# Optimization experiments

Hardware: AMD Instinct MI355X
Metric: run time of the kernel (lower is better)

Reference implementation:

```python
import jax, jax.numpy as jnp
import numpy as np

WIN = (7, 7, 7)
N = WIN[0] * WIN[1] * WIN[2]   # 343 tokens per window
DIM = 192
NH = 6
HD = DIM // NH                  # 32
B = 128                         # batch * num_windows


def _relative_position_index():
    # exact replica of the torch buffer computation
    coords = np.stack(np.meshgrid(np.arange(WIN[0]), np.arange(WIN[1]), np.arange(WIN[2]), indexing='ij'))
    cf = coords.reshape(3, -1)                       # [3, N]
    rel = cf[:, :, None] - cf[:, None, :]            # [3, N, N]
    rel = rel.transpose(1, 2, 0).astype(np.int64)    # [N, N, 3]
    rel[..., 0] += WIN[0] - 1
    rel[..., 1] += WIN[1] - 1
    rel[..., 2] += WIN[2] - 1
    rel[..., 0] *= (2 * WIN[1] - 1) * (2 * WIN[2] - 1)
    rel[..., 1] *= (2 * WIN[2] - 1)
    return rel.sum(-1).astype(np.int32)              # [N, N]


def setup_inputs() -> dict:
    key = jax.random.key(0)
    k = jax.random.split(key, 8)
    table_size = (2 * WIN[0] - 1) * (2 * WIN[1] - 1) * (2 * WIN[2] - 1)  # 2197
    return {
        'x':        jax.random.normal(k[0], (B, N, DIM), jnp.float32),
        'x_1':      jax.random.normal(k[1], (B, N, DIM), jnp.float32),
        'qkv_w':    jax.random.normal(k[2], (3 * DIM, DIM), jnp.float32) * 0.02,
        'qkv_b':    jnp.zeros((3 * DIM,), jnp.float32),
        'proj_w':   jax.random.normal(k[3], (DIM, DIM), jnp.float32) * 0.02,
        'proj_b':   jnp.zeros((DIM,), jnp.float32),
        'rpb_table': jax.random.normal(k[4], (table_size, NH), jnp.float32) * 0.02,
        'rel_idx':  jnp.asarray(_relative_position_index()),
    }


def reference(x, x_1, qkv_w, qkv_b, proj_w, proj_b, rpb_table, rel_idx):
    scale = HD ** -0.5

    def qkv_proj(t):
        # [B, N, 3C] -> [3, B, nH, N, hd]
        q = (t @ qkv_w.T + qkv_b).reshape(B, N, 3, NH, HD).transpose(2, 0, 3, 1, 4)
        return q[0], q[1], q[2]

    qx, kx, vx = qkv_proj(x)
    q1, k1, v1 = qkv_proj(x_1)

    # gathered relative-position bias: [1, nH, N, N]
    bias = rpb_table[rel_idx.reshape(-1)].reshape(N, N, NH).transpose(2, 0, 1)[None]

    def attend(q, k, v):
        a = jnp.einsum('bhnd,bhmd->bhnm', q * scale, k) + bias
        a = jax.nn.softmax(a, axis=-1)
        o = jnp.einsum('bhnm,bhmd->bhnd', a, v).transpose(0, 2, 1, 3).reshape(B, N, DIM)
        return o @ proj_w.T + proj_b

    # cross-modal pairing: q from x with k,v from x_1; q from x_1 with k,v from x
    out = attend(qx, k1, v1)
    out_1 = attend(q1, kx, vx)
    return out, out_1
```

## Files before the change

kernel.cpp:

```cpp
#include <hip/hip_runtime.h>
#include <hip/hip_bf16.h>

#define BW 128
#define NTOK 343
#define DIMC 192
#define NHEAD 6
#define HDIM 32
#define TOK (BW * NTOK)
#define M2 (2 * TOK)
#define NN (NTOK * NTOK)
#define BSTR 344
#define BNN (NTOK * BSTR)
#define QSCALE 0.17677669529663687f
#define LOG2E 1.4426950408889634f

typedef unsigned int uint32;
typedef __attribute__((ext_vector_type(8))) short short8;
typedef __attribute__((ext_vector_type(4))) float f32x4;

__device__ __forceinline__ unsigned short f2bf(float f) {
  uint32 u = __float_as_uint(f);
  u += 0x7fffu + ((u >> 16) & 1u);
  return (unsigned short)(u >> 16);
}

__device__ __forceinline__ uint32 pkpair(float a, float b) {
  __hip_bfloat162 h = __float22bfloat162_rn(make_float2(a, b));
  uint32 u;
  __builtin_memcpy(&u, &h, 4);
  return u;
}

__device__ __forceinline__ uint4 pack8bf(const float4 a, const float4 b) {
  uint4 pk;
  pk.x = pkpair(a.x, a.y);
  pk.y = pkpair(a.z, a.w);
  pk.z = pkpair(b.x, b.y);
  pk.w = pkpair(b.z, b.w);
  return pk;
}

__device__ __forceinline__ float fexp2(float x) {
  float r;
  asm("v_exp_f32 %0, %1" : "=v"(r) : "v"(x));
  return r;
}

__global__ void k_bias(const float* __restrict__ rpb, const int* __restrict__ ridx,
                       float* __restrict__ biasws) {
  const int idx = blockIdx.x * 256 + threadIdx.x;
  if (idx < NN) {
    const int r = ridx[idx];
    const int i = idx / NTOK, j = idx % NTOK;
#pragma unroll
    for (int h = 0; h < NHEAD; ++h)
      biasws[h * BNN + i * BSTR + j] = rpb[r * NHEAD + h] * LOG2E;
  }
}

__global__ __launch_bounds__(256) void k_qkv(const float* __restrict__ x,
                                             const float* __restrict__ x1,
                                             const float* __restrict__ w,
                                             const float* __restrict__ bvec,
                                             unsigned short* __restrict__ qkvo) {
  __shared__ unsigned short Xs[128][200];
  __shared__ unsigned short Ws[64][200];
  const int R0 = blockIdx.x * 128;
  const int s = R0 / TOK;
  const int tokbase = R0 % TOK;
  const float* __restrict__ src = s ? x1 : x;
  const int tid = threadIdx.x;
  const int lane = tid & 63, wv = tid >> 6;
  const int c16 = lane & 15, q4 = lane >> 4;
  const int wr = wv >> 1, wc = wv & 1;

  int bidxv[4], nnv[4];
#pragma unroll
  for (int n = 0; n < 4; ++n) {
    const int tok = tokbase + wr * 64 + n * 16 + c16;
    bidxv[n] = tok / NTOK;
    nnv[n] = tok % NTOK;
  }

  for (int c = tid; c < 128 * 24; c += 256) {
    const int r = c / 24, k8 = (c % 24) * 8;
    const float* p = &src[(size_t)(tokbase + r) * DIMC + k8];
    const float4 a = *reinterpret_cast<const float4*>(p);
    const float4 b = *reinterpret_cast<const float4*>(p + 4);
    *reinterpret_cast<uint4*>(&Xs[r][k8]) = pack8bf(a, b);
  }

  float4 wa[6], wb[6];
#pragma unroll
  for (int i = 0; i < 6; ++i) {
    const int c = tid + i * 256;
    const int r = c / 24, k8 = (c % 24) * 8;
    const float* p = &w[(size_t)(0 * 64 + r) * DIMC + k8];
    wa[i] = *reinterpret_cast<const float4*>(p);
    wb[i] = *reinterpret_cast<const float4*>(p + 4);
  }

  for (int ct = 0; ct < 9; ++ct) {
    __syncthreads();
#pragma unroll
    for (int i = 0; i < 6; ++i) {
      const int c = tid + i * 256;
      const int r = c / 24, k8 = (c % 24) * 8;
      *reinterpret_cast<uint4*>(&Ws[r][k8]) = pack8bf(wa[i], wb[i]);
    }
    __syncthreads();

    if (ct < 8) {
#pragma unroll
      for (int i = 0; i < 6; ++i) {
        const int c = tid + i * 256;
        const int r = c / 24, k8 = (c % 24) * 8;
        const float* p = &w[(size_t)((ct + 1) * 64 + r) * DIMC + k8];
        wa[i] = *reinterpret_cast<const float4*>(p);
        wb[i] = *reinterpret_cast<const float4*>(p + 4);
      }
    }

    const int colbase = ct * 64 + wc * 32;
    f32x4 acc[2][4];
#pragma unroll
    for (int m = 0; m < 2; ++m) {
      const float4 bb = *reinterpret_cast<const float4*>(&bvec[colbase + m * 16 + q4 * 4]);
#pragma unroll
      for (int n = 0; n < 4; ++n) acc[m][n] = f32x4{bb.x, bb.y, bb.z, bb.w};
    }
#pragma unroll
    for (int ks = 0; ks < 6; ++ks) {
      const short8 w0 = *reinterpret_cast<const short8*>(&Ws[wc * 32 + c16][ks * 32 + q4 * 8]);
      const short8 w1 = *reinterpret_cast<const short8*>(&Ws[wc * 32 + 16 + c16][ks * 32 + q4 * 8]);
      short8 xf[4];
#pragma unroll
      for (int n = 0; n < 4; ++n)
        xf[n] = *reinterpret_cast<const short8*>(&Xs[wr * 64 + n * 16 + c16][ks * 32 + q4 * 8]);
#pragma unroll
      for (int n = 0; n < 4; ++n) {
        acc[0][n] = __builtin_amdgcn_mfma_f32_16x16x32_bf16(w0, xf[n], acc[0][n], 0, 0, 0);
        acc[1][n] = __builtin_amdgcn_mfma_f32_16x16x32_bf16(w1, xf[n], acc[1][n], 0, 0, 0);
      }
    }

    const int t = ct / 3;
    const float qs = (t == 0) ? (QSCALE * LOG2E) : 1.0f;
#pragma unroll
    for (int m = 0; m < 2; ++m) {
      const int col0 = colbase + m * 16 + q4 * 4;
      const int h = (col0 - t * DIMC) / HDIM;
      const int d0 = col0 & (HDIM - 1);
      const size_t hb = ((size_t)(s * 3 + t) * BW) * NHEAD + h;
#pragma unroll
      for (int n = 0; n < 4; ++n) {
        const f32x4 a = acc[m][n];
        uint2 pk;
        pk.x = pkpair(a[0] * qs, a[1] * qs);
        pk.y = pkpair(a[2] * qs, a[3] * qs);
        const size_t ob = ((hb + (size_t)bidxv[n] * NHEAD) * NTOK + nnv[n]) * HDIM + d0;
        *reinterpret_cast<uint2*>(&qkvo[ob]) = pk;
      }
    }
  }
}

__global__ __launch_bounds__(256) void k_attn(const __hip_bfloat16* __restrict__ qkvi,
                                              const float* __restrict__ biasws,
                                              __hip_bfloat16* __restrict__ Ows) {
  __shared__ unsigned short Ks[352][40];
  __shared__ unsigned short Vt[32][360];
  const int bid = blockIdx.x;
  const int h = bid / (2 * BW);
  const int sb = bid % (2 * BW);
  const int s = sb >> 7;
  const int b = sb & 127;
  const int so = 1 - s;
  const size_t qbase = (((size_t)(s * 3 + 0) * BW + b) * NHEAD + h) * (size_t)NTOK * HDIM;
  const size_t kbase = (((size_t)(so * 3 + 1) * BW + b) * NHEAD + h) * (size_t)NTOK * HDIM;
  const size_t vbase = (((size_t)(so * 3 + 2) * BW + b) * NHEAD + h) * (size_t)NTOK * HDIM;
  const unsigned short* __restrict__ qp = (const unsigned short*)qkvi;
  unsigned short* __restrict__ op = (unsigned short*)Ows;
  const float* __restrict__ bh = biasws + (size_t)h * BNN;
  const int tid = threadIdx.x;

  for (int idx = tid; idx < 352 * 4; idx += 256) {
    const int n = idx >> 2, d0 = (idx & 3) * 8;
    uint4 v = {0u, 0u, 0u, 0u};
    if (n < NTOK) v = *reinterpret_cast<const uint4*>(qp + kbase + (size_t)n * HDIM + d0);
    *reinterpret_cast<uint4*>(&Ks[n][d0]) = v;
  }
  for (int idx = tid; idx < NTOK * 4; idx += 256) {
    const int n = idx >> 2, d0 = (idx & 3) * 8;
    const uint4 v = *reinterpret_cast<const uint4*>(qp + vbase + (size_t)n * HDIM + d0);
    const unsigned short* ep = reinterpret_cast<const unsigned short*>(&v);
#pragma unroll
    for (int e = 0; e < 8; ++e) Vt[d0 + e][n] = ep[e];
  }
  for (int idx = tid; idx < 32 * 9; idx += 256) Vt[idx / 9][NTOK + idx % 9] = 0;
  __syncthreads();

  const int lane = tid & 63, w = tid >> 6;
  const int c16 = lane & 15, q4 = lane >> 4;
  const bool loSel = (q4 < 2);

  for (int qt = w; qt < 22; qt += 4) {
    const int iq = qt * 16 + c16;
    const int iqc = (iq < NTOK) ? iq : NTOK - 1;
    const short8 qf = *reinterpret_cast<const short8*>(qp + qbase + (size_t)iqc * HDIM + q4 * 8);
    const float* brow = bh + (size_t)iqc * BSTR;

    f32x4 o0 = {0.f, 0.f, 0.f, 0.f}, o1 = {0.f, 0.f, 0.f, 0.f};
    float mA, sumA;

    {
      f32x4 acc[12];
#pragma unroll
      for (int kt = 0; kt < 12; ++kt) {
        const float4 bv = *reinterpret_cast<const float4*>(brow + kt * 16 + q4 * 4);
        acc[kt] = f32x4{bv.x, bv.y, bv.z, bv.w};
      }
#pragma unroll
      for (int kt = 0; kt < 12; ++kt) {
        const short8 kf = *reinterpret_cast<const short8*>(&Ks[kt * 16 + c16][q4 * 8]);
        acc[kt] = __builtin_amdgcn_mfma_f32_16x16x32_bf16(kf, qf, acc[kt], 0, 0, 0);
      }
      float m = acc[0][0];
#pragma unroll
      for (int kt = 0; kt < 12; ++kt)
#pragma unroll
        for (int r = 0; r < 4; ++r) m = fmaxf(m, acc[kt][r]);
      m = fmaxf(m, __shfl_xor(m, 16, 64));
      m = fmaxf(m, __shfl_xor(m, 32, 64));
      mA = m;
      float sum = 0.f;
#pragma unroll
      for (int kt = 0; kt < 12; ++kt)
#pragma unroll
        for (int r = 0; r < 4; ++r) {
          const float p = fexp2(acc[kt][r] - m);
          acc[kt][r] = p;
          sum += p;
        }
      sumA = sum;

#pragma unroll
      for (int ks = 0; ks < 6; ++ks) {
        uint4 pw;
        pw.x = pkpair(acc[2 * ks][0], acc[2 * ks][1]);
        pw.y = pkpair(acc[2 * ks][2], acc[2 * ks][3]);
        pw.z = pkpair(acc[2 * ks + 1][0], acc[2 * ks + 1][1]);
        pw.w = pkpair(acc[2 * ks + 1][2], acc[2 * ks + 1][3]);
        const short8 pf = *reinterpret_cast<const short8*>(&pw);
        const uint2 v0lo = *reinterpret_cast<const uint2*>(&Vt[c16][ks * 32 + q4 * 4]);
        const uint2 v0hi = *reinterpret_cast<const uint2*>(&Vt[c16][ks * 32 + 16 + q4 * 4]);
        const uint2 v1lo = *reinterpret_cast<const uint2*>(&Vt[16 + c16][ks * 32 + q4 * 4]);
        const uint2 v1hi = *reinterpret_cast<const uint2*>(&Vt[16 + c16][ks * 32 + 16 + q4 * 4]);
        uint4 vw0, vw1;
        vw0.x = v0lo.x; vw0.y = v0lo.y; vw0.z = v0hi.x; vw0.w = v0hi.y;
        vw1.x = v1lo.x; vw1.y = v1lo.y; vw1.z = v1hi.x; vw1.w = v1hi.y;
        const short8 v0 = *reinterpret_cast<const short8*>(&vw0);
        const short8 v1 = *reinterpret_cast<const short8*>(&vw1);
        o0 = __builtin_amdgcn_mfma_f32_16x16x32_bf16(pf, v0, o0, 0, 0, 0);
        o1 = __builtin_amdgcn_mfma_f32_16x16x32_bf16(pf, v1, o1, 0, 0, 0);
      }
    }

    float rinv;
    {
      f32x4 acc[10];
#pragma unroll
      for (int k2 = 0; k2 < 10; ++k2) {
        const int kt = 12 + k2;
        const int jb = (kt < 21) ? (kt * 16 + q4 * 4) : (336 + (loSel ? q4 * 4 : 0));
        const float4 bv = *reinterpret_cast<const float4*>(brow + jb);
        acc[k2] = f32x4{bv.x, bv.y, bv.z, bv.w};
      }
#pragma unroll
      for (int k2 = 0; k2 < 10; ++k2) {
        const short8 kf = *reinterpret_cast<const short8*>(&Ks[(12 + k2) * 16 + c16][q4 * 8]);
        acc[k2] = __builtin_amdgcn_mfma_f32_16x16x32_bf16(kf, qf, acc[k2], 0, 0, 0);
      }
#pragma unroll
      for (int r = 0; r < 4; ++r)
        if (q4 * 4 + r >= 7) acc[9][r] = -1e30f;

      float m = acc[0][0];
#pragma unroll
      for (int k2 = 0; k2 < 10; ++k2)
#pragma unroll
        for (int r = 0; r < 4; ++r) m = fmaxf(m, acc[k2][r]);
      m = fmaxf(m, __shfl_xor(m, 16, 64));
      m = fmaxf(m, __shfl_xor(m, 32, 64));
      m = fmaxf(m, mA);
      const float alpha = fexp2(mA - m);

      float sum = 0.f;
#pragma unroll
      for (int k2 = 0; k2 < 10; ++k2)
#pragma unroll
        for (int r = 0; r < 4; ++r) {
          const float p = fexp2(acc[k2][r] - m);
          acc[k2][r] = p;
          sum += p;
        }
      float lanesum = sumA * alpha + sum;
      lanesum += __shfl_xor(lanesum, 16, 64);
      lanesum += __shfl_xor(lanesum, 32, 64);
      rinv = 1.f / lanesum;

      float alphar[4];
#pragma unroll
      for (int r = 0; r < 4; ++r) alphar[r] = __shfl(alpha, q4 * 4 + r, 64);
#pragma unroll
      for (int r = 0; r < 4; ++r) {
        o0[r] *= alphar[r];
        o1[r] *= alphar[r];
      }

#pragma unroll
      for (int ks = 6; ks < 11; ++ks) {
        const int k2 = 2 * (ks - 6);
        uint4 pw;
        pw.x = pkpair(acc[k2][0], acc[k2][1]);
        pw.y = pkpair(acc[k2][2], acc[k2][3]);
        pw.z = pkpair(acc[k2 + 1][0], acc[k2 + 1][1]);
        pw.w = pkpair(acc[k2 + 1][2], acc[k2 + 1][3]);
        const short8 pf = *reinterpret_cast<const short8*>(&pw);
        const uint2 v0lo = *reinterpret_cast<const uint2*>(&Vt[c16][ks * 32 + q4 * 4]);
        const uint2 v0hi = *reinterpret_cast<const uint2*>(&Vt[c16][ks * 32 + 16 + q4 * 4]);
        const uint2 v1lo = *reinterpret_cast<const uint2*>(&Vt[16 + c16][ks * 32 + q4 * 4]);
        const uint2 v1hi = *reinterpret_cast<const uint2*>(&Vt[16 + c16][ks * 32 + 16 + q4 * 4]);
        uint4 vw0, vw1;
        vw0.x = v0lo.x; vw0.y = v0lo.y; vw0.z = v0hi.x; vw0.w = v0hi.y;
        vw1.x = v1lo.x; vw1.y = v1lo.y; vw1.z = v1hi.x; vw1.w = v1hi.y;
        const short8 v0 = *reinterpret_cast<const short8*>(&vw0);
        const short8 v1 = *reinterpret_cast<const short8*>(&vw1);
        o0 = __builtin_amdgcn_mfma_f32_16x16x32_bf16(pf, v0, o0, 0, 0, 0);
        o1 = __builtin_amdgcn_mfma_f32_16x16x32_bf16(pf, v1, o1, 0, 0, 0);
      }
    }

    float rsv[4];
#pragma unroll
    for (int r = 0; r < 4; ++r) rsv[r] = __shfl(rinv, q4 * 4 + r, 64);
#pragma unroll
    for (int r = 0; r < 4; ++r) {
      const int i = qt * 16 + q4 * 4 + r;
      if (i < NTOK) {
        const size_t ob = ((size_t)s * TOK + (size_t)b * NTOK + i) * DIMC + h * HDIM;
        op[ob + c16]      = f2bf(o0[r] * rsv[r]);
        op[ob + 16 + c16] = f2bf(o1[r] * rsv[r]);
      }
    }
  }
}

__global__ __launch_bounds__(256) void k_proj(const unsigned short* __restrict__ Oin,
                                              const float* __restrict__ w,
                                              const float* __restrict__ pb,
                                              float* __restrict__ out) {
  __shared__ unsigned short Xs[64][200];
  __shared__ unsigned short Ws[64][200];
  const int R0 = blockIdx.x * 64;
  const int tid = threadIdx.x;
  const int lane = tid & 63, wv = tid >> 6;
  const int c16 = lane & 15, q4 = lane >> 4;
  const int wr = wv >> 1, wc = wv & 1;

  for (int c = tid; c < 64 * 24; c += 256) {
    const int r = c / 24, k8 = (c % 24) * 8;
    *reinterpret_cast<uint4*>(&Xs[r][k8]) =
        *reinterpret_cast<const uint4*>(&Oin[(size_t)(R0 + r) * DIMC + k8]);
  }

  for (int ct = 0; ct < 3; ++ct) {
    __syncthreads();
    for (int c = tid; c < 64 * 24; c += 256) {
      const int r = c / 24, k8 = (c % 24) * 8;
      const float* p = &w[(size_t)(ct * 64 + r) * DIMC + k8];
      const float4 a = *reinterpret_cast<const float4*>(p);
      const float4 b = *reinterpret_cast<const float4*>(p + 4);
      *reinterpret_cast<uint4*>(&Ws[r][k8]) = pack8bf(a, b);
    }
    __syncthreads();

    const int colbase = ct * 64 + wc * 32;
    f32x4 acc[2][2];
#pragma unroll
    for (int m = 0; m < 2; ++m) {
      const float4 bb = *reinterpret_cast<const float4*>(&pb[colbase + m * 16 + q4 * 4]);
      acc[m][0] = f32x4{bb.x, bb.y, bb.z, bb.w};
      acc[m][1] = f32x4{bb.x, bb.y, bb.z, bb.w};
    }
#pragma unroll
    for (int ks = 0; ks < 6; ++ks) {
      const short8 x0 = *reinterpret_cast<const short8*>(&Xs[wr * 32 + c16][ks * 32 + q4 * 8]);
      const short8 x1f = *reinterpret_cast<const short8*>(&Xs[wr * 32 + 16 + c16][ks * 32 + q4 * 8]);
      const short8 w0 = *reinterpret_cast<const short8*>(&Ws[wc * 32 + c16][ks * 32 + q4 * 8]);
      const short8 w1 = *reinterpret_cast<const short8*>(&Ws[wc * 32 + 16 + c16][ks * 32 + q4 * 8]);
      acc[0][0] = __builtin_amdgcn_mfma_f32_16x16x32_bf16(w0, x0, acc[0][0], 0, 0, 0);
      acc[0][1] = __builtin_amdgcn_mfma_f32_16x16x32_bf16(w0, x1f, acc[0][1], 0, 0, 0);
      acc[1][0] = __builtin_amdgcn_mfma_f32_16x16x32_bf16(w1, x0, acc[1][0], 0, 0, 0);
      acc[1][1] = __builtin_amdgcn_mfma_f32_16x16x32_bf16(w1, x1f, acc[1][1], 0, 0, 0);
    }

#pragma unroll
    for (int m = 0; m < 2; ++m) {
      const int col0 = colbase + m * 16 + q4 * 4;
#pragma unroll
      for (int n = 0; n < 2; ++n) {
        const int row = R0 + wr * 32 + n * 16 + c16;
        float4 ov;
        ov.x = acc[m][n][0];
        ov.y = acc[m][n][1];
        ov.z = acc[m][n][2];
        ov.w = acc[m][n][3];
        *reinterpret_cast<float4*>(&out[(size_t)row * DIMC + col0]) = ov;
      }
    }
  }
}

extern "C" void kernel_launch(void* const* d_in, const int* in_sizes, int n_in,
                              void* d_out, int out_size, void* d_ws, size_t ws_size,
                              hipStream_t stream) {
  const float* x      = (const float*)d_in[0];
  const float* x1     = (const float*)d_in[1];
  const float* qkv_w  = (const float*)d_in[2];
  const float* qkv_b  = (const float*)d_in[3];
  const float* proj_w = (const float*)d_in[4];
  const float* proj_b = (const float*)d_in[5];
  const float* rpb    = (const float*)d_in[6];
  const int*   ridx   = (const int*)d_in[7];
  float* out = (float*)d_out;

  char* ws = (char*)d_ws;
  unsigned short* qkv  = (unsigned short*)ws;
  unsigned short* Ows  = (unsigned short*)(ws + 101154816);
  float*          bws  = (float*)(ws + 101154816 + 33718272);

  k_bias<<<(NN + 255) / 256, 256, 0, stream>>>(rpb, ridx, bws);
  k_qkv<<<M2 / 128, 256, 0, stream>>>(x, x1, qkv_w, qkv_b, qkv);
  k_attn<<<2 * BW * NHEAD, 256, 0, stream>>>((const __hip_bfloat16*)qkv, bws,
                                             (__hip_bfloat16*)Ows);
  k_proj<<<M2 / 64, 256, 0, stream>>>(Ows, proj_w, proj_b, out);
}
```

Measured before the change: 176.6 us.

## Read K fragments directly from global and permute V layout in LDS

```diff
diff --git a/kernel.cpp b/kernel.cpp
--- a/kernel.cpp
+++ b/kernel.cpp
@@ -44,6 +44,11 @@
   float r;
   asm("v_exp_f32 %0, %1" : "=v"(r) : "v"(x));
   return r;
+}
+
+__device__ __forceinline__ int vperm(int n) {
+  const int base = n & ~31, l = n & 31, lo = l & 15, hi = l >> 4;
+  return base + ((lo >> 2) << 3) + (hi << 2) + (lo & 3);
 }
 
 __global__ void k_bias(const float* __restrict__ rpb, const int* __restrict__ ridx,
@@ -95,7 +100,7 @@
   for (int i = 0; i < 6; ++i) {
     const int c = tid + i * 256;
     const int r = c / 24, k8 = (c % 24) * 8;
-    const float* p = &w[(size_t)(0 * 64 + r) * DIMC + k8];
+    const float* p = &w[(size_t)r * DIMC + k8];
     wa[i] = *reinterpret_cast<const float4*>(p);
     wb[i] = *reinterpret_cast<const float4*>(p + 4);
   }
@@ -168,7 +173,6 @@
 __global__ __launch_bounds__(256) void k_attn(const __hip_bfloat16* __restrict__ qkvi,
                                               const float* __restrict__ biasws,
                                               __hip_bfloat16* __restrict__ Ows) {
-  __shared__ unsigned short Ks[352][40];
   __shared__ unsigned short Vt[32][360];
   const int bid = blockIdx.x;
   const int h = bid / (2 * BW);
@@ -184,25 +188,22 @@
   const float* __restrict__ bh = biasws + (size_t)h * BNN;
   const int tid = threadIdx.x;
 
-  for (int idx = tid; idx < 352 * 4; idx += 256) {
-    const int n = idx >> 2, d0 = (idx & 3) * 8;
-    uint4 v = {0u, 0u, 0u, 0u};
-    if (n < NTOK) v = *reinterpret_cast<const uint4*>(qp + kbase + (size_t)n * HDIM + d0);
-    *reinterpret_cast<uint4*>(&Ks[n][d0]) = v;
-  }
   for (int idx = tid; idx < NTOK * 4; idx += 256) {
     const int n = idx >> 2, d0 = (idx & 3) * 8;
+    const int np = vperm(n);
     const uint4 v = *reinterpret_cast<const uint4*>(qp + vbase + (size_t)n * HDIM + d0);
     const unsigned short* ep = reinterpret_cast<const unsigned short*>(&v);
 #pragma unroll
-    for (int e = 0; e < 8; ++e) Vt[d0 + e][n] = ep[e];
-  }
-  for (int idx = tid; idx < 32 * 9; idx += 256) Vt[idx / 9][NTOK + idx % 9] = 0;
+    for (int e = 0; e < 8; ++e) Vt[d0 + e][np] = ep[e];
+  }
+  for (int idx = tid; idx < 32 * 9; idx += 256)
+    Vt[idx / 9][vperm(NTOK + idx % 9)] = 0;
   __syncthreads();
 
   const int lane = tid & 63, w = tid >> 6;
   const int c16 = lane & 15, q4 = lane >> 4;
   const bool loSel = (q4 < 2);
+  const unsigned short* __restrict__ kp = qp + kbase + c16 * HDIM + q4 * 8;
 
   for (int qt = w; qt < 22; qt += 4) {
     const int iq = qt * 16 + c16;
@@ -222,7 +223,7 @@
       }
 #pragma unroll
       for (int kt = 0; kt < 12; ++kt) {
-        const short8 kf = *reinterpret_cast<const short8*>(&Ks[kt * 16 + c16][q4 * 8]);
+        const short8 kf = *reinterpret_cast<const short8*>(kp + (size_t)kt * 16 * HDIM);
         acc[kt] = __builtin_amdgcn_mfma_f32_16x16x32_bf16(kf, qf, acc[kt], 0, 0, 0);
       }
       float m = acc[0][0];
@@ -252,15 +253,8 @@
         pw.z = pkpair(acc[2 * ks + 1][0], acc[2 * ks + 1][1]);
         pw.w = pkpair(acc[2 * ks + 1][2], acc[2 * ks + 1][3]);
         const short8 pf = *reinterpret_cast<const short8*>(&pw);
-        const uint2 v0lo = *reinterpret_cast<const uint2*>(&Vt[c16][ks * 32 + q4 * 4]);
-        const uint2 v0hi = *reinterpret_cast<const uint2*>(&Vt[c16][ks * 32 + 16 + q4 * 4]);
-        const uint2 v1lo = *reinterpret_cast<const uint2*>(&Vt[16 + c16][ks * 32 + q4 * 4]);
-        const uint2 v1hi = *reinterpret_cast<const uint2*>(&Vt[16 + c16][ks * 32 + 16 + q4 * 4]);
-        uint4 vw0, vw1;
-        vw0.x = v0lo.x; vw0.y = v0lo.y; vw0.z = v0hi.x; vw0.w = v0hi.y;
-        vw1.x = v1lo.x; vw1.y = v1lo.y; vw1.z = v1hi.x; vw1.w = v1hi.y;
-        const short8 v0 = *reinterpret_cast<const short8*>(&vw0);
-        const short8 v1 = *reinterpret_cast<const short8*>(&vw1);
+        const short8 v0 = *reinterpret_cast<const short8*>(&Vt[c16][ks * 32 + q4 * 8]);
+        const short8 v1 = *reinterpret_cast<const short8*>(&Vt[16 + c16][ks * 32 + q4 * 8]);
         o0 = __builtin_amdgcn_mfma_f32_16x16x32_bf16(pf, v0, o0, 0, 0, 0);
         o1 = __builtin_amdgcn_mfma_f32_16x16x32_bf16(pf, v1, o1, 0, 0, 0);
       }
@@ -278,7 +272,7 @@
       }
 #pragma unroll
       for (int k2 = 0; k2 < 10; ++k2) {
-        const short8 kf = *reinterpret_cast<const short8*>(&Ks[(12 + k2) * 16 + c16][q4 * 8]);
+        const short8 kf = *reinterpret_cast<const short8*>(kp + (size_t)(12 + k2) * 16 * HDIM);
         acc[k2] = __builtin_amdgcn_mfma_f32_16x16x32_bf16(kf, qf, acc[k2], 0, 0, 0);
       }
 #pragma unroll
@@ -327,15 +321,8 @@
         pw.z = pkpair(acc[k2 + 1][0], acc[k2 + 1][1]);
         pw.w = pkpair(acc[k2 + 1][2], acc[k2 + 1][3]);
         const short8 pf = *reinterpret_cast<const short8*>(&pw);
-        const uint2 v0lo = *reinterpret_cast<const uint2*>(&Vt[c16][ks * 32 + q4 * 4]);
-        const uint2 v0hi = *reinterpret_cast<const uint2*>(&Vt[c16][ks * 32 + 16 + q4 * 4]);
-        const uint2 v1lo = *reinterpret_cast<const uint2*>(&Vt[16 + c16][ks * 32 + q4 * 4]);
-        const uint2 v1hi = *reinterpret_cast<const uint2*>(&Vt[16 + c16][ks * 32 + 16 + q4 * 4]);
-        uint4 vw0, vw1;
-        vw0.x = v0lo.x; vw0.y = v0lo.y; vw0.z = v0hi.x; vw0.w = v0hi.y;
-        vw1.x = v1lo.x; vw1.y = v1lo.y; vw1.z = v1hi.x; vw1.w = v1hi.y;
-        const short8 v0 = *reinterpret_cast<const short8*>(&vw0);
-        const short8 v1 = *reinterpret_cast<const short8*>(&vw1);
+        const short8 v0 = *reinterpret_cast<const short8*>(&Vt[c16][ks * 32 + q4 * 8]);
+        const short8 v1 = *reinterpret_cast<const short8*>(&Vt[16 + c16][ks * 32 + q4 * 8]);
         o0 = __builtin_amdgcn_mfma_f32_16x16x32_bf16(pf, v0, o0, 0, 0, 0);
         o1 = __builtin_amdgcn_mfma_f32_16x16x32_bf16(pf, v1, o1, 0, 0, 0);
       }
```

New measurement: 196.1 us. 11.1% more time.
